# Performance work log

Measured on AMD Instinct MI355X. Metric: run time of the kernel, lower is better.

## Reference

```python
import jax, jax.numpy as jnp
import numpy as np

D_MODEL = 1024
N_HEADS = 16
HEAD_DIM = D_MODEL // N_HEADS
B, L = 2, 2048


def setup_inputs() -> dict:
    key = jax.random.key(0)
    ks = jax.random.split(key, 9)
    s = 1.0 / np.sqrt(D_MODEL)
    return {
        "hidden_states": jax.random.normal(ks[0], (B, L, D_MODEL), dtype=jnp.float32),
        "Wq": jax.random.uniform(ks[1], (D_MODEL, D_MODEL), jnp.float32, -s, s),
        "bq": jax.random.uniform(ks[2], (D_MODEL,), jnp.float32, -s, s),
        "Wk": jax.random.uniform(ks[3], (D_MODEL, D_MODEL), jnp.float32, -s, s),
        "bk": jax.random.uniform(ks[4], (D_MODEL,), jnp.float32, -s, s),
        "Wv": jax.random.uniform(ks[5], (D_MODEL, D_MODEL), jnp.float32, -s, s),
        "bv": jax.random.uniform(ks[6], (D_MODEL,), jnp.float32, -s, s),
        "Wo": jax.random.uniform(ks[7], (D_MODEL, D_MODEL), jnp.float32, -s, s),
        "bo": jax.random.uniform(ks[8], (D_MODEL,), jnp.float32, -s, s),
    }


def reference(hidden_states, Wq, bq, Wk, bk, Wv, bv, Wo, bo):
    b, l, d = hidden_states.shape
    h, hd = N_HEADS, HEAD_DIM
    scale = jnp.sqrt(jnp.asarray(hd, hidden_states.dtype))
    # projections (weights stored as [in, out], equivalent to torch Linear W.T)
    Q = (hidden_states @ Wq + bq).reshape(b, l, h, hd).transpose(0, 2, 1, 3)
    K = (hidden_states @ Wk + bk).reshape(b, l, h, hd).transpose(0, 2, 1, 3)
    V = (hidden_states @ Wv + bv).reshape(b, l, h, hd).transpose(0, 2, 1, 3)
    # [b, h, l, l] scores with causal mask
    scores = jnp.einsum("bhqd,bhkd->bhqk", Q, K) / scale
    causal = jnp.tril(jnp.ones((l, l), dtype=bool))
    scores = jnp.where(causal, scores, jnp.asarray(-jnp.inf, scores.dtype))
    weights = jax.nn.softmax(scores, axis=-1)
    out = jnp.einsum("bhqk,bhkd->bhqd", weights, V)
    out = out.transpose(0, 2, 1, 3).reshape(b, l, d)
    return out @ Wo + bo
```

## Files before the change

### kernel.cpp

```cpp
#include <hip/hip_runtime.h>

typedef unsigned short u16;
typedef unsigned int u32;
typedef __attribute__((ext_vector_type(8))) short bf16x8;
typedef __attribute__((ext_vector_type(4))) float f32x4;

__device__ __forceinline__ u16 f2bf(float f) {
    union { float f; u32 u; } x; x.f = f;
    u32 r = x.u + 0x7FFFu + ((x.u >> 16) & 1u);
    return (u16)(r >> 16);
}

__device__ __forceinline__ u16 f2bf_fast(float f) {
    union { float f; u32 u; } x; x.f = f;
    return (u16)((x.u + 0x8000u) >> 16);
}

__device__ __forceinline__ void gload16(const u16* g, u16* l) {
    __builtin_amdgcn_global_load_lds(
        (const __attribute__((address_space(1))) void*)g,
        (__attribute__((address_space(3))) void*)l,
        16, 0, 0);
}

__device__ __forceinline__ f32x4 mfma16(bf16x8 a, bf16x8 b, f32x4 c) {
    return __builtin_amdgcn_mfma_f32_16x16x32_bf16(a, b, c, 0, 0, 0);
}


__global__ __launch_bounds__(256) void cvt_x(const float* __restrict__ in, u16* __restrict__ out, int n4) {
    int i = blockIdx.x * blockDim.x + threadIdx.x;
    if (i >= n4) return;
    float4 v = ((const float4*)in)[i];
    u16* o = out + (size_t)i * 4;
    o[0] = f2bf(v.x); o[1] = f2bf(v.y); o[2] = f2bf(v.z); o[3] = f2bf(v.w);
}

__global__ __launch_bounds__(256) void transpose_w4(const float* __restrict__ Wq, const float* __restrict__ Wk,
                                                    const float* __restrict__ Wv, const float* __restrict__ Wo,
                                                    u16* __restrict__ qkvt, u16* __restrict__ wot) {
    __shared__ float tile[32][33];
    const float* in;
    u16* out;
    if (blockIdx.z == 0)      { in = Wq; out = qkvt; }
    else if (blockIdx.z == 1) { in = Wk; out = qkvt + 1024 * 1024; }
    else if (blockIdx.z == 2) { in = Wv; out = qkvt + 2 * 1024 * 1024; }
    else                      { in = Wo; out = wot; }
    const int bx = blockIdx.x * 32, by = blockIdx.y * 32;
    const int tx = threadIdx.x & 31, ty4 = (threadIdx.x >> 5) * 4;
#pragma unroll
    for (int j = 0; j < 4; ++j)
        tile[ty4 + j][tx] = in[(size_t)(by + ty4 + j) * 1024 + bx + tx];
    __syncthreads();
#pragma unroll
    for (int j = 0; j < 4; ++j)
        out[(size_t)(bx + ty4 + j) * 1024 + by + tx] = f2bf(tile[tx][ty4 + j]);
}

__global__ __launch_bounds__(256) void pack_bias(const float* __restrict__ bq, const float* __restrict__ bk,
                                                 const float* __restrict__ bv, float* __restrict__ out) {
    int i = blockIdx.x * blockDim.x + threadIdx.x;
    if (i >= 3072) return;
    out[i] = (i < 1024) ? bq[i] : ((i < 2048) ? bk[i - 1024] : bv[i - 2048]);
}

template<int MODE>
__global__ __launch_bounds__(256) void gemm128(const u16* __restrict__ A, const u16* __restrict__ Bt,
                                               const float* __restrict__ bias,
                                               u16* __restrict__ oq, u16* __restrict__ ok, u16* __restrict__ ov,
                                               float* __restrict__ of, int K)
{
    __shared__ u16 As[128 * 32];
    __shared__ u16 Bs[128 * 32];

    const int n0 = blockIdx.x * 128;
    const int m0 = blockIdx.y * 128;
    const int t = threadIdx.x;
    const int w = t >> 6, lane = t & 63;
    const int g = lane >> 4, lr = lane & 15;
    const int wm = w >> 1, wn = w & 1;
    const int srow = lane >> 2;
    const int scol = (lane & 3) * 8;

    f32x4 acc[4][4] = {};

    for (int k0 = 0; k0 < K; k0 += 32) {
        __syncthreads();
#pragma unroll
        for (int i = 0; i < 2; ++i) {
            const int c = w + i * 4;
            const int mrow = c * 16 + srow;
            gload16(A  + (size_t)(m0 + mrow) * K + k0 + scol, &As[c * 512 + lane * 8]);
            gload16(Bt + (size_t)(n0 + mrow) * K + k0 + scol, &Bs[c * 512 + lane * 8]);
        }
        __syncthreads();
        bf16x8 af[4], bfr[4];
#pragma unroll
        for (int mi = 0; mi < 4; ++mi) af[mi]  = *(const bf16x8*)&As[(wm * 64 + mi * 16 + lr) * 32 + g * 8];
#pragma unroll
        for (int ni = 0; ni < 4; ++ni) bfr[ni] = *(const bf16x8*)&Bs[(wn * 64 + ni * 16 + lr) * 32 + g * 8];
#pragma unroll
        for (int mi = 0; mi < 4; ++mi)
#pragma unroll
            for (int ni = 0; ni < 4; ++ni)
                acc[mi][ni] = mfma16(af[mi], bfr[ni], acc[mi][ni]);
    }

#pragma unroll
    for (int mi = 0; mi < 4; ++mi) {
#pragma unroll
        for (int ni = 0; ni < 4; ++ni) {
            const int col = n0 + wn * 64 + ni * 16 + lr;
            const int row0 = m0 + wm * 64 + mi * 16 + g * 4;
            const float bs = bias[col];
            if (MODE == 0) {
                const int mat = col >> 10;
                const int nn = col & 1023;
                const int h = nn >> 6, d = nn & 63;
#pragma unroll
                for (int j = 0; j < 4; ++j) {
                    const int rr = row0 + j;
                    const int b = rr >> 11, ll = rr & 2047;
                    const int bh = b * 16 + h;
                    const float v = acc[mi][ni][j] + bs;
                    if (mat == 0)      oq[((size_t)bh * 2048 + ll) * 64 + d] = f2bf(v * 0.1803368801111244f);
                    else if (mat == 1) ok[((size_t)bh * 2048 + ll) * 64 + d] = f2bf(v);
                    else               ov[((size_t)bh * 64 + d) * 2048 + ll] = f2bf(v);
                }
            } else {
#pragma unroll
                for (int j = 0; j < 4; ++j) {
                    const int rr = row0 + j;
                    of[(size_t)rr * 1024 + col] = acc[mi][ni][j] + bs;
                }
            }
        }
    }
}

__global__ __launch_bounds__(256) void attn(const u16* __restrict__ Q, const u16* __restrict__ Kg,
                                            const u16* __restrict__ Vt, u16* __restrict__ O)
{
    __shared__ u16 Ks[2][64 * 64];
    __shared__ u16 Vs[2][64 * 64];
    __shared__ u16 Ps[4][16 * 64];

    const int bh = blockIdx.x;
    const int qb = (int)gridDim.y - 1 - blockIdx.y;
    const int q0 = qb * 64;
    const int t = threadIdx.x;
    const int w = t >> 6, lane = t & 63;
    const int g = lane >> 4, lr = lane & 15;
    const int qw = q0 + w * 16;
    const int sw = lr & 7;

    const u16* Qb = Q  + (size_t)bh * 2048 * 64;
    const u16* Kb = Kg + (size_t)bh * 2048 * 64;
    const u16* Vb = Vt + (size_t)bh * 64 * 2048;

    const bf16x8 qf0 = *(const bf16x8*)&Qb[(size_t)(qw + lr) * 64 + g * 8];
    const bf16x8 qf1 = *(const bf16x8*)&Qb[(size_t)(qw + lr) * 64 + 32 + g * 8];

    const short one = (short)0x3F80;
    const bf16x8 vones = {one, one, one, one, one, one, one, one};

    f32x4 oacc[4] = {};
    f32x4 lsacc = {};
    float mrun = -1e30f;

    int bpaddr[4];
#pragma unroll
    for (int j = 0; j < 4; ++j) bpaddr[j] = (20 * g + j) * 4;

    const int pw_base = lr * 64;
    const int g2h = g >> 1;
    const int wic2 = (2 * g) & 3;

    bf16x8 kreg[2], vreg[2];
    const int srow0 = t >> 3, sch = t & 7;
    auto issue = [&](int kb) {
#pragma unroll
        for (int i = 0; i < 2; ++i) {
            const int row = srow0 + i * 32;
            kreg[i] = *(const bf16x8*)&Kb[(size_t)(kb * 64 + row) * 64 + sch * 8];
            vreg[i] = *(const bf16x8*)&Vb[(size_t)row * 2048 + kb * 64 + sch * 8];
        }
    };
    auto commit = [&](int buf) {
#pragma unroll
        for (int i = 0; i < 2; ++i) {
            const int row = srow0 + i * 32;
            const int chs = sch ^ (row & 7);
            *(bf16x8*)&Ks[buf][row * 64 + chs * 8] = kreg[i];
            *(bf16x8*)&Vs[buf][row * 64 + chs * 8] = vreg[i];
        }
    };

    issue(0);
    commit(0);

    for (int kb = 0; kb <= qb; ++kb) {
        const int cur = kb & 1;
        const int k0 = kb * 64;
        __syncthreads();
        const bool more = (kb < qb);
        if (more) issue(kb + 1);

        f32x4 s[4] = {};
        __builtin_amdgcn_s_setprio(1);
#pragma unroll
        for (int ni = 0; ni < 4; ++ni) {
            const int row = ni * 16 + lr;
            bf16x8 kf0 = *(const bf16x8*)&Ks[cur][row * 64 + (g ^ sw) * 8];
            bf16x8 kf1 = *(const bf16x8*)&Ks[cur][row * 64 + ((4 + g) ^ sw) * 8];
            s[ni] = mfma16(kf0, qf0, s[ni]);
            s[ni] = mfma16(kf1, qf1, s[ni]);
        }
        __builtin_amdgcn_s_setprio(0);

        if (kb == qb) {
            const int qq = qw + lr;
#pragma unroll
            for (int ni = 0; ni < 4; ++ni)
#pragma unroll
                for (int j = 0; j < 4; ++j)
                    if (k0 + ni * 16 + g * 4 + j > qq) s[ni][j] = -1e30f;
        }

        float pm = fmaxf(fmaxf(fmaxf(s[0][0], s[0][1]), fmaxf(s[0][2], s[0][3])),
                         fmaxf(fmaxf(s[1][0], s[1][1]), fmaxf(s[1][2], s[1][3])));
        pm = fmaxf(pm, fmaxf(fmaxf(fmaxf(s[2][0], s[2][1]), fmaxf(s[2][2], s[2][3])),
                             fmaxf(fmaxf(s[3][0], s[3][1]), fmaxf(s[3][2], s[3][3]))));
        pm = fmaxf(pm, __shfl_xor(pm, 16));
        pm = fmaxf(pm, __shfl_xor(pm, 32));

        if (__any(pm > mrun + 8.f)) {
            const float mn = fmaxf(mrun, pm);
            const float r = __builtin_amdgcn_exp2f(mrun - mn);
            mrun = mn;
            const int ri = __float_as_int(r);
#pragma unroll
            for (int j = 0; j < 4; ++j) {
                const float ro = __int_as_float(__builtin_amdgcn_ds_bpermute(bpaddr[j], ri));
                lsacc[j] *= ro;
#pragma unroll
                for (int df = 0; df < 4; ++df) oacc[df][j] *= ro;
            }
        }

#pragma unroll
        for (int ni = 0; ni < 4; ++ni) {
            const int c8 = 2 * ni + g2h;
#pragma unroll
            for (int jp = 0; jp < 2; ++jp) {
                const float plo = __builtin_amdgcn_exp2f(s[ni][2 * jp]     - mrun);
                const float phi = __builtin_amdgcn_exp2f(s[ni][2 * jp + 1] - mrun);
                const u32 pr = (u32)f2bf_fast(plo) | ((u32)f2bf_fast(phi) << 16);
                const int wic = wic2 + jp;
                *(u32*)&Ps[w][pw_base + (c8 ^ sw) * 8 + wic * 2] = pr;
            }
        }

        if (more) commit(cur ^ 1);

        const bf16x8 p0 = *(const bf16x8*)&Ps[w][lr * 64 + (g ^ sw) * 8];
        const bf16x8 p1 = *(const bf16x8*)&Ps[w][lr * 64 + ((4 + g) ^ sw) * 8];
        __builtin_amdgcn_s_setprio(1);
        lsacc = mfma16(p0, vones, lsacc);
        lsacc = mfma16(p1, vones, lsacc);
#pragma unroll
        for (int df = 0; df < 4; ++df) {
            const int row = df * 16 + lr;
            bf16x8 vf0 = *(const bf16x8*)&Vs[cur][row * 64 + (g ^ sw) * 8];
            bf16x8 vf1 = *(const bf16x8*)&Vs[cur][row * 64 + ((4 + g) ^ sw) * 8];
            oacc[df] = mfma16(p0, vf0, oacc[df]);
            oacc[df] = mfma16(p1, vf1, oacc[df]);
        }
        __builtin_amdgcn_s_setprio(0);
    }

    const int b = bh >> 4, h = bh & 15;
#pragma unroll
    for (int j = 0; j < 4; ++j) {
        const float inv = 1.f / lsacc[j];
        const int l = qw + g * 4 + j;
#pragma unroll
        for (int df = 0; df < 4; ++df)
            O[((size_t)b * 2048 + l) * 1024 + h * 64 + df * 16 + lr] = f2bf(oacc[df][j] * inv);
    }
}


extern "C" void kernel_launch(void* const* d_in, const int* in_sizes, int n_in,
                              void* d_out, int out_size, void* d_ws, size_t ws_size,
                              hipStream_t stream)
{
    const float* hs = (const float*)d_in[0];
    const float* Wq = (const float*)d_in[1];
    const float* bq = (const float*)d_in[2];
    const float* Wk = (const float*)d_in[3];
    const float* bk = (const float*)d_in[4];
    const float* Wv = (const float*)d_in[5];
    const float* bv = (const float*)d_in[6];
    const float* Wo = (const float*)d_in[7];
    const float* bo = (const float*)d_in[8];
    float* out = (float*)d_out;

    char* ws = (char*)d_ws;
    u16*   Xbf   = (u16*)(ws);
    u16*   Wqkvt = (u16*)(ws + (8ull  << 20));
    u16*   Wot   = (u16*)(ws + (14ull << 20));
    float* bqkv  = (float*)(ws + (16ull << 20));
    u16*   Qbuf  = (u16*)(ws + (17ull << 20));
    u16*   Kbuf  = (u16*)(ws + (25ull << 20));
    u16*   Vtbuf = (u16*)(ws + (33ull << 20));
    u16*   Abuf  = Xbf;

    cvt_x<<<4096, 256, 0, stream>>>(hs, Xbf, 4096 * 1024 / 4);
    transpose_w4<<<dim3(32, 32, 4), 256, 0, stream>>>(Wq, Wk, Wv, Wo, Wqkvt, Wot);
    pack_bias<<<12, 256, 0, stream>>>(bq, bk, bv, bqkv);

    gemm128<0><<<dim3(24, 32), 256, 0, stream>>>(Xbf, Wqkvt, bqkv, Qbuf, Kbuf, Vtbuf, nullptr, 1024);
    attn<<<dim3(32, 32), 256, 0, stream>>>(Qbuf, Kbuf, Vtbuf, Abuf);
    gemm128<1><<<dim3(8, 32), 256, 0, stream>>>(Abuf, Wot, bo, nullptr, nullptr, nullptr, out, 1024);
}
```

Baseline: 134.9 us.

## Split long causal query blocks across two KV halves and merge partials

Query blocks in the upper half of the causal attention (qb>=16) are each split into two work items covering the lower and upper halves of their key range. Partial unnormalized outputs, running max and row sums are written to fp32 workspace, and a new merge kernel combines them. The goal is to balance per-block work and cut the tail latency from the longest causal blocks. The cost is an extra kernel launch plus fp32 partial writes and reads. The split path only runs when the workspace is large enough.

Result: no change. 135.8 us (+0.7%).

```diff
diff --git a/kernel.cpp b/kernel.cpp
--- a/kernel.cpp
+++ b/kernel.cpp
@@ -139,14 +139,30 @@
 }
 
 __global__ __launch_bounds__(256) void attn(const u16* __restrict__ Q, const u16* __restrict__ Kg,
-                                            const u16* __restrict__ Vt, u16* __restrict__ O)
+                                            const u16* __restrict__ Vt, u16* __restrict__ O,
+                                            float* __restrict__ Opart, float* __restrict__ Mp,
+                                            float* __restrict__ Lp, int do_split)
 {
     __shared__ u16 Ks[2][64 * 64];
     __shared__ u16 Vs[2][64 * 64];
     __shared__ u16 Ps[4][16 * 64];
 
     const int bh = blockIdx.x;
-    const int qb = (int)gridDim.y - 1 - blockIdx.y;
+    int qb, k_lo, k_hi, split;
+    if (!do_split) {
+        qb = 31 - (int)blockIdx.y; k_lo = 0; k_hi = qb + 1; split = -1;
+    } else {
+        const int y = (int)blockIdx.y;
+        if (y < 32) {
+            qb = 16 + (y >> 1);
+            split = y & 1;
+            const int mid = (qb + 1) >> 1;
+            k_lo = split ? mid : 0;
+            k_hi = split ? qb + 1 : mid;
+        } else {
+            qb = 47 - y; k_lo = 0; k_hi = qb + 1; split = -1;
+        }
+    }
     const int q0 = qb * 64;
     const int t = threadIdx.x;
     const int w = t >> 6, lane = t & 63;
@@ -196,14 +212,14 @@
         }
     };
 
-    issue(0);
+    issue(k_lo);
     commit(0);
 
-    for (int kb = 0; kb <= qb; ++kb) {
-        const int cur = kb & 1;
+    for (int kb = k_lo; kb < k_hi; ++kb) {
+        const int cur = (kb - k_lo) & 1;
         const int k0 = kb * 64;
         __syncthreads();
-        const bool more = (kb < qb);
+        const bool more = (kb + 1 < k_hi);
         if (more) issue(kb + 1);
 
         f32x4 s[4] = {};
@@ -279,15 +295,55 @@
         __builtin_amdgcn_s_setprio(0);
     }
 
+    if (split < 0) {
+        const int b = bh >> 4, h = bh & 15;
+#pragma unroll
+        for (int j = 0; j < 4; ++j) {
+            const float inv = 1.f / lsacc[j];
+            const int l = qw + g * 4 + j;
+#pragma unroll
+            for (int df = 0; df < 4; ++df)
+                O[((size_t)b * 2048 + l) * 1024 + h * 64 + df * 16 + lr] = f2bf(oacc[df][j] * inv);
+        }
+    } else {
+        float* Ob = Opart + ((size_t)split * 32 + bh) * (1024 * 64);
+        const int rb = qw - 1024 + 4 * g;
+#pragma unroll
+        for (int j = 0; j < 4; ++j)
+#pragma unroll
+            for (int df = 0; df < 4; ++df)
+                Ob[(size_t)(rb + j) * 64 + df * 16 + lr] = oacc[df][j];
+        if (lr == 0) {
+#pragma unroll
+            for (int j = 0; j < 4; ++j)
+                Lp[(split * 32 + bh) * 1024 + rb + j] = lsacc[j];
+        }
+        if (g == 0)
+            Mp[(split * 32 + bh) * 1024 + (qw - 1024) + lr] = mrun;
+    }
+}
+
+__global__ __launch_bounds__(256) void attn_merge(const float* __restrict__ Opart,
+                                                  const float* __restrict__ Mp,
+                                                  const float* __restrict__ Lp,
+                                                  u16* __restrict__ O)
+{
+    const int idx = blockIdx.x * 256 + threadIdx.x;
+    const int d  = idx & 63;
+    const int rr = (idx >> 6) & 1023;
+    const int bh = idx >> 16;
+    const int si = bh * 1024 + rr;
+    const float m0 = Mp[si], m1 = Mp[32 * 1024 + si];
+    const float l0 = Lp[si], l1 = Lp[32 * 1024 + si];
+    const float M  = fmaxf(m0, m1);
+    const float w0 = __builtin_amdgcn_exp2f(m0 - M);
+    const float w1 = __builtin_amdgcn_exp2f(m1 - M);
+    const float o0 = Opart[(size_t)si * 64 + d];
+    const float o1 = Opart[(size_t)(32 * 1024 + si) * 64 + d];
+    const float o  = (w0 * o0 + w1 * o1) / (w0 * l0 + w1 * l1);
     const int b = bh >> 4, h = bh & 15;
-#pragma unroll
-    for (int j = 0; j < 4; ++j) {
-        const float inv = 1.f / lsacc[j];
-        const int l = qw + g * 4 + j;
-#pragma unroll
-        for (int df = 0; df < 4; ++df)
-            O[((size_t)b * 2048 + l) * 1024 + h * 64 + df * 16 + lr] = f2bf(oacc[df][j] * inv);
-    }
+    const int r = 1024 + rr;
+    O[((size_t)b * 2048 + r) * 1024 + h * 64 + d] = f2bf(o);
 }
 
 
@@ -315,12 +371,24 @@
     u16*   Kbuf  = (u16*)(ws + (25ull << 20));
     u16*   Vtbuf = (u16*)(ws + (33ull << 20));
     u16*   Abuf  = Xbf;
+    float* Opart = (float*)(ws + (42ull << 20));
+    float* Mpart = (float*)(ws + (58ull << 20));
+    float* Lpart = (float*)(ws + (58ull << 20) + (512ull << 10));
+
+    const int do_split = (ws_size >= (59ull << 20)) ? 1 : 0;
 
     cvt_x<<<4096, 256, 0, stream>>>(hs, Xbf, 4096 * 1024 / 4);
     transpose_w4<<<dim3(32, 32, 4), 256, 0, stream>>>(Wq, Wk, Wv, Wo, Wqkvt, Wot);
     pack_bias<<<12, 256, 0, stream>>>(bq, bk, bv, bqkv);
 
     gemm128<0><<<dim3(24, 32), 256, 0, stream>>>(Xbf, Wqkvt, bqkv, Qbuf, Kbuf, Vtbuf, nullptr, 1024);
-    attn<<<dim3(32, 32), 256, 0, stream>>>(Qbuf, Kbuf, Vtbuf, Abuf);
+
+    if (do_split) {
+        attn<<<dim3(32, 48), 256, 0, stream>>>(Qbuf, Kbuf, Vtbuf, Abuf, Opart, Mpart, Lpart, 1);
+        attn_merge<<<8192, 256, 0, stream>>>(Opart, Mpart, Lpart, Abuf);
+    } else {
+        attn<<<dim3(32, 32), 256, 0, stream>>>(Qbuf, Kbuf, Vtbuf, Abuf, nullptr, nullptr, nullptr, 0);
+    }
+
     gemm128<1><<<dim3(8, 32), 256, 0, stream>>>(Abuf, Wot, bo, nullptr, nullptr, nullptr, out, 1024);
 }
```
